# Performance work log

Hardware: AMD Instinct MI355X
Metric: run time of the kernel (lower is better)

Reference implementation:

```python
import jax, jax.numpy as jnp
import numpy as np

DIM = 256
MUL = 4
NUM_ENTRIES = 64
B, K = 16, 64
R = MUL * DIM


def setup_inputs() -> dict:
    key = jax.random.key(0)
    k_slots, k_idx, k_w1, k_w2 = jax.random.split(key, 4)
    slots = jax.random.normal(k_slots, (B, K, DIM), dtype=jnp.float32)
    indices = jax.random.randint(k_idx, (B, K), 0, NUM_ENTRIES, dtype=jnp.int64)
    # xavier_normal: std = sqrt(2 / (fan_in + fan_out)) over last two dims
    std1 = float(np.sqrt(2.0 / (DIM + R)))
    std2 = float(np.sqrt(2.0 / (R + DIM)))
    w1 = jax.random.normal(k_w1, (NUM_ENTRIES, DIM, R), dtype=jnp.float32) * std1
    w2 = jax.random.normal(k_w2, (NUM_ENTRIES, R, DIM), dtype=jnp.float32) * std2
    b1 = jnp.zeros((NUM_ENTRIES, R), dtype=jnp.float32)
    b2 = jnp.zeros((NUM_ENTRIES, DIM), dtype=jnp.float32)
    return {"slots": slots, "w1": w1, "b1": b1, "w2": w2, "b2": b2, "indices": indices}


def reference(slots, w1, b1, w2, b2, indices):
    # gather per-(b,k) expert weights, then 2-layer MLP (matvec per slot)
    h = jnp.einsum('bkd,bkdr->bkr', slots, w1[indices]) + b1[indices]  # (B,K,R)
    h = jax.nn.relu(h)
    out = jnp.einsum('bkr,bkrd->bkd', h, w2[indices]) + b2[indices]    # (B,K,DIM)
    return out
```

## Files before the change

### kernel.cpp

```cpp
#include <hip/hip_runtime.h>
#include <stdint.h>

#define DIMC 256
#define RTOT 1024
#define NE 64
#define NSLOT 1024
#define RCN 8
#define RCW 128
#define TILE 32
#define XSTR 264
#define NT 16

typedef short bfrag __attribute__((ext_vector_type(8)));
typedef float f32x4 __attribute__((ext_vector_type(4)));

#define VMCNT(N) asm volatile("s_waitcnt vmcnt(" #N ")" ::: "memory")
#define LGKM0_BAR()                                          \
  do {                                                       \
    asm volatile("s_waitcnt lgkmcnt(0)" ::: "memory");       \
    __builtin_amdgcn_s_barrier();                            \
  } while (0)

static __device__ __forceinline__ unsigned short f2bf(float f) {
  unsigned u = __float_as_uint(f);
  return (unsigned short)((u + 0x7FFFu + ((u >> 16) & 1u)) >> 16);
}

static __device__ __forceinline__ bfrag pack8(const float* f) {
  union { unsigned short u[8]; bfrag v; } r;
#pragma unroll
  for (int i = 0; i < 8; ++i) r.u[i] = f2bf(f[i]);
  return r.v;
}

static __device__ __forceinline__ void gload16(const float* g, float* l) {
  __builtin_amdgcn_global_load_lds(
      (const __attribute__((address_space(1))) void*)g,
      (__attribute__((address_space(3))) void*)l, 16, 0, 0);
}

template <int USE_WS>
__global__ __launch_bounds__(512, 4) void mlp_kernel(
    const float* __restrict__ slots, const float* __restrict__ w1,
    const float* __restrict__ b1, const float* __restrict__ w2,
    const float* __restrict__ b2, const int* __restrict__ indices,
    float* __restrict__ part, float* __restrict__ out) {
  const int e  = blockIdx.x;
  const int rc = blockIdx.y;
  const int t  = threadIdx.x;
  const int l  = t & 63;
  const int w  = t >> 6;
  const int ln = l & 15;
  const int kg = l >> 4;
  const int rbase = rc * RCW;

  __shared__ __align__(16) float WT[3][4096];
  __shared__ __align__(16) unsigned short X[TILE * XSTR];
  __shared__ unsigned short blist[NSLOT];
  __shared__ int sid[TILE];
  __shared__ int bn_s;

  if (t == 0) bn_s = 0;
  __syncthreads();
  {
    int i0 = indices[t] & (NE - 1);
    int i1 = indices[t + 512] & (NE - 1);
    if (i0 == e) { int p = atomicAdd(&bn_s, 1); blist[p] = (unsigned short)t; }
    if (i1 == e) { int p = atomicAdd(&bn_s, 1); blist[p] = (unsigned short)(t + 512); }
  }
  __syncthreads();
  const int n = bn_s;
  if (n == 0) return;

  const float* w1e = w1 + (size_t)e * DIMC * RTOT + rbase;
  const float* w2e = w2 + (size_t)e * RTOT * DIMC + (size_t)rbase * DIMC;
  const int   c    = w * 16 + ln;
  const float b1v  = b1[e * RTOT + rbase + c];
  float* prc = part + (size_t)rc * NSLOT * DIMC;

  auto STAGE = [&](int tt, float* buf) {
    if (tt < 8) {
      const float* g = w1e + (size_t)(tt * 32 + (t >> 5)) * RTOT + (t & 31) * 4;
      gload16(g, buf + t * 4);
      gload16(g + (size_t)16 * RTOT, buf + 2048 + t * 4);
    } else {
      const int rt = (tt - 8) >> 1, dh = tt & 1;
      const float* g =
          w2e + (size_t)(rt * 32 + (t >> 5)) * DIMC + dh * 128 + (t & 31) * 4;
      gload16(g, buf + t * 4);
      gload16(g + 16 * DIMC, buf + 2048 + t * 4);
    }
  };

  for (int s0 = 0; s0 < n; s0 += TILE) {
    const int m = (n - s0 < TILE) ? (n - s0) : TILE;

    LGKM0_BAR();
    if (t < TILE) sid[t] = (t < m) ? (int)blist[s0 + t] : 0;
    LGKM0_BAR();

#pragma unroll
    for (int i = t; i < TILE * 64; i += 512) {
      int s = i >> 6, d4 = (i & 63) * 4;
      float4 v = make_float4(0.f, 0.f, 0.f, 0.f);
      if (s < m) v = ((const float4*)slots)[(size_t)sid[s] * 64 + (i & 63)];
      union { unsigned short u[4]; uint2 q; } p;
      p.u[0] = f2bf(v.x); p.u[1] = f2bf(v.y);
      p.u[2] = f2bf(v.z); p.u[3] = f2bf(v.w);
      *(uint2*)&X[s * XSTR + d4] = p.q;
    }

    f32x4 acc1[2];
    acc1[0] = (f32x4)(0.f); acc1[1] = (f32x4)(0.f);
    f32x4 acc2[2][2];
#pragma unroll
    for (int mt = 0; mt < 2; ++mt)
#pragma unroll
      for (int dh = 0; dh < 2; ++dh) acc2[mt][dh] = (f32x4)(0.f);

    STAGE(0, WT[0]);
    STAGE(1, WT[1]);

#pragma unroll
    for (int tt = 0; tt < NT; ++tt) {
      if (tt < NT - 1) VMCNT(2);
      else             VMCNT(0);
      LGKM0_BAR();

      if (tt == 8) {
#pragma unroll
        for (int mt = 0; mt < 2; ++mt)
#pragma unroll
          for (int reg = 0; reg < 4; ++reg) {
            float h = fmaxf(acc1[mt][reg] + b1v, 0.f);
            X[(mt * 16 + kg * 4 + reg) * XSTR + c] = f2bf(h);
          }
        LGKM0_BAR();
      }

      if (tt + 2 < NT) STAGE(tt + 2, WT[(tt + 2) % 3]);

      {
        const float* buf = WT[tt % 3];
        float f[8];
#pragma unroll
        for (int j = 0; j < 8; ++j) f[j] = buf[(kg * 8 + j) * RCW + c];
        bfrag b = pack8(f);
        if (tt < 8) {
          bfrag a0 = *(const bfrag*)&X[ln * XSTR + tt * 32 + kg * 8];
          bfrag a1 = *(const bfrag*)&X[(16 + ln) * XSTR + tt * 32 + kg * 8];
          acc1[0] = __builtin_amdgcn_mfma_f32_16x16x32_bf16(a0, b, acc1[0], 0, 0, 0);
          acc1[1] = __builtin_amdgcn_mfma_f32_16x16x32_bf16(a1, b, acc1[1], 0, 0, 0);
        } else {
          const int rt = (tt - 8) >> 1, dh = tt & 1;
          bfrag a0 = *(const bfrag*)&X[ln * XSTR + rt * 32 + kg * 8];
          bfrag a1 = *(const bfrag*)&X[(16 + ln) * XSTR + rt * 32 + kg * 8];
          acc2[0][dh] = __builtin_amdgcn_mfma_f32_16x16x32_bf16(a0, b, acc2[0][dh], 0, 0, 0);
          acc2[1][dh] = __builtin_amdgcn_mfma_f32_16x16x32_bf16(a1, b, acc2[1][dh], 0, 0, 0);
        }
      }
    }

#pragma unroll
    for (int dh = 0; dh < 2; ++dh) {
      const int col = dh * 128 + c;
      const float b2v =
          (!USE_WS && rc == 0) ? b2[e * DIMC + col] : 0.f;
#pragma unroll
      for (int mt = 0; mt < 2; ++mt)
#pragma unroll
        for (int reg = 0; reg < 4; ++reg) {
          const int row = mt * 16 + kg * 4 + reg;
          if (row < m) {
            if (USE_WS) {
              prc[(size_t)sid[row] * DIMC + col] = acc2[mt][dh][reg];
            } else {
              atomicAdd(&out[(size_t)sid[row] * DIMC + col],
                        acc2[mt][dh][reg] + b2v);
            }
          }
        }
    }
  }
}

__global__ __launch_bounds__(256) void reduce_kernel(
    const float* __restrict__ part, const float* __restrict__ b2,
    const int* __restrict__ indices, float* __restrict__ out) {
  const int i = blockIdx.x * 256 + threadIdx.x;
  const int slot = i >> 6;
  const int e = indices[slot] & (NE - 1);
  f32x4 s = *(const f32x4*)(b2 + e * DIMC + (i & 63) * 4);
#pragma unroll
  for (int rc = 0; rc < RCN; ++rc)
    s += *(const f32x4*)(part + (size_t)rc * NSLOT * DIMC + (size_t)i * 4);
  *(f32x4*)(out + (size_t)i * 4) = s;
}

extern "C" void kernel_launch(void* const* d_in, const int* in_sizes, int n_in,
                              void* d_out, int out_size, void* d_ws, size_t ws_size,
                              hipStream_t stream) {
  const float* slots   = (const float*)d_in[0];
  const float* w1      = (const float*)d_in[1];
  const float* b1      = (const float*)d_in[2];
  const float* w2      = (const float*)d_in[3];
  const float* b2      = (const float*)d_in[4];
  const int*   indices = (const int*)d_in[5];
  float* out = (float*)d_out;

  const size_t need = (size_t)RCN * NSLOT * DIMC * sizeof(float);
  if (ws_size >= need) {
    float* part = (float*)d_ws;
    mlp_kernel<1><<<dim3(NE, RCN), 512, 0, stream>>>(slots, w1, b1, w2, b2,
                                                     indices, part, out);
    reduce_kernel<<<NSLOT * DIMC / 4 / 256, 256, 0, stream>>>(part, b2,
                                                              indices, out);
  } else {
    hipMemsetAsync(d_out, 0, (size_t)out_size * sizeof(float), stream);
    mlp_kernel<0><<<dim3(NE, RCN), 512, 0, stream>>>(slots, w1, b1, w2, b2,
                                                     indices, nullptr, out);
  }
}
```

Baseline: 163.2 us.

## Give each wave private weight staging with all loads issued upfront

Replaces the block-wide triple-buffered weight pipeline, which needed a barrier at every step, with a per-wave 16 KB LDS region. Each wave issues all of its w1 loads at once (and later all of its w2 loads) and waits on them with graded vmcnt counts, so block barriers are only needed around the X and hidden-activation exchanges. The layer-2 column split also changes so that each wave owns 32 output columns. LDS grows from 48 KB to 128 KB of weight buffers and the occupancy hint drops from 4 to 2, which trades latency hiding across blocks for deeper in-flight loads within each wave.

```diff
diff --git a/kernel.cpp b/kernel.cpp
--- a/kernel.cpp
+++ b/kernel.cpp
@@ -9,12 +9,11 @@
 #define RCW 128
 #define TILE 32
 #define XSTR 264
-#define NT 16
 
 typedef short bfrag __attribute__((ext_vector_type(8)));
 typedef float f32x4 __attribute__((ext_vector_type(4)));
 
-#define VMCNT(N) asm volatile("s_waitcnt vmcnt(" #N ")" ::: "memory")
+#define WAITV(n) asm volatile("s_waitcnt vmcnt(" #n ")" ::: "memory")
 #define LGKM0_BAR()                                          \
   do {                                                       \
     asm volatile("s_waitcnt lgkmcnt(0)" ::: "memory");       \
@@ -39,8 +38,23 @@
       (__attribute__((address_space(3))) void*)l, 16, 0, 0);
 }
 
+static __device__ __forceinline__ void waitv_l1(int ks) {
+  switch (ks) {
+    case 0: WAITV(14); break; case 1: WAITV(12); break;
+    case 2: WAITV(10); break; case 3: WAITV(8);  break;
+    case 4: WAITV(6);  break; case 5: WAITV(4);  break;
+    case 6: WAITV(2);  break; default: WAITV(0); break;
+  }
+}
+static __device__ __forceinline__ void waitv_l2(int rt) {
+  switch (rt) {
+    case 0: WAITV(12); break; case 1: WAITV(8); break;
+    case 2: WAITV(4);  break; default: WAITV(0); break;
+  }
+}
+
 template <int USE_WS>
-__global__ __launch_bounds__(512, 4) void mlp_kernel(
+__global__ __launch_bounds__(512, 2) void mlp_kernel(
     const float* __restrict__ slots, const float* __restrict__ w1,
     const float* __restrict__ b1, const float* __restrict__ w2,
     const float* __restrict__ b2, const int* __restrict__ indices,
@@ -54,7 +68,7 @@
   const int kg = l >> 4;
   const int rbase = rc * RCW;
 
-  __shared__ __align__(16) float WT[3][4096];
+  __shared__ __align__(16) float WB[8][4096];
   __shared__ __align__(16) unsigned short X[TILE * XSTR];
   __shared__ unsigned short blist[NSLOT];
   __shared__ int sid[TILE];
@@ -76,28 +90,18 @@
   const float* w2e = w2 + (size_t)e * RTOT * DIMC + (size_t)rbase * DIMC;
   const int   c    = w * 16 + ln;
   const float b1v  = b1[e * RTOT + rbase + c];
+  float* WBw = WB[w];
   float* prc = part + (size_t)rc * NSLOT * DIMC;
 
-  auto STAGE = [&](int tt, float* buf) {
-    if (tt < 8) {
-      const float* g = w1e + (size_t)(tt * 32 + (t >> 5)) * RTOT + (t & 31) * 4;
-      gload16(g, buf + t * 4);
-      gload16(g + (size_t)16 * RTOT, buf + 2048 + t * 4);
-    } else {
-      const int rt = (tt - 8) >> 1, dh = tt & 1;
-      const float* g =
-          w2e + (size_t)(rt * 32 + (t >> 5)) * DIMC + dh * 128 + (t & 31) * 4;
-      gload16(g, buf + t * 4);
-      gload16(g + 16 * DIMC, buf + 2048 + t * 4);
-    }
-  };
+  const int r4 = l >> 2, c4 = (l & 3) * 4;
+  const int r8 = l >> 3, c8 = (l & 7) * 4;
 
   for (int s0 = 0; s0 < n; s0 += TILE) {
     const int m = (n - s0 < TILE) ? (n - s0) : TILE;
 
-    LGKM0_BAR();
+    __syncthreads();
     if (t < TILE) sid[t] = (t < m) ? (int)blist[s0 + t] : 0;
-    LGKM0_BAR();
+    __syncthreads();
 
 #pragma unroll
     for (int i = t; i < TILE * 64; i += 512) {
@@ -109,63 +113,79 @@
       p.u[2] = f2bf(v.z); p.u[3] = f2bf(v.w);
       *(uint2*)&X[s * XSTR + d4] = p.q;
     }
+    __syncthreads();
+
+#pragma unroll
+    for (int ks = 0; ks < 8; ++ks)
+#pragma unroll
+      for (int hf = 0; hf < 2; ++hf) {
+        const float* src =
+            w1e + (size_t)(ks * 32 + hf * 16 + r4) * RTOT + w * 16 + c4;
+        gload16(src, WBw + ks * 512 + hf * 256 + l * 4);
+      }
 
     f32x4 acc1[2];
     acc1[0] = (f32x4)(0.f); acc1[1] = (f32x4)(0.f);
+#pragma unroll
+    for (int ks = 0; ks < 8; ++ks) {
+      waitv_l1(ks);
+      float f[8];
+#pragma unroll
+      for (int j = 0; j < 8; ++j) f[j] = WBw[ks * 512 + (kg * 8 + j) * 16 + ln];
+      bfrag b = pack8(f);
+      bfrag a0 = *(const bfrag*)&X[ln * XSTR + ks * 32 + kg * 8];
+      bfrag a1 = *(const bfrag*)&X[(16 + ln) * XSTR + ks * 32 + kg * 8];
+      acc1[0] = __builtin_amdgcn_mfma_f32_16x16x32_bf16(a0, b, acc1[0], 0, 0, 0);
+      acc1[1] = __builtin_amdgcn_mfma_f32_16x16x32_bf16(a1, b, acc1[1], 0, 0, 0);
+    }
+
+    asm volatile("s_waitcnt lgkmcnt(0)" ::: "memory");
+#pragma unroll
+    for (int rt = 0; rt < 4; ++rt)
+#pragma unroll
+      for (int q = 0; q < 4; ++q) {
+        const float* src =
+            w2e + (size_t)(rt * 32 + q * 8 + r8) * DIMC + w * 32 + c8;
+        gload16(src, WBw + rt * 1024 + q * 256 + l * 4);
+      }
+
+    LGKM0_BAR();
+
+#pragma unroll
+    for (int mt = 0; mt < 2; ++mt)
+#pragma unroll
+      for (int reg = 0; reg < 4; ++reg) {
+        float h = fmaxf(acc1[mt][reg] + b1v, 0.f);
+        X[(mt * 16 + kg * 4 + reg) * XSTR + c] = f2bf(h);
+      }
+    LGKM0_BAR();
+
     f32x4 acc2[2][2];
 #pragma unroll
     for (int mt = 0; mt < 2; ++mt)
 #pragma unroll
-      for (int dh = 0; dh < 2; ++dh) acc2[mt][dh] = (f32x4)(0.f);
-
-    STAGE(0, WT[0]);
-    STAGE(1, WT[1]);
-
-#pragma unroll
-    for (int tt = 0; tt < NT; ++tt) {
-      if (tt < NT - 1) VMCNT(2);
-      else             VMCNT(0);
-      LGKM0_BAR();
-
-      if (tt == 8) {
-#pragma unroll
-        for (int mt = 0; mt < 2; ++mt)
-#pragma unroll
-          for (int reg = 0; reg < 4; ++reg) {
-            float h = fmaxf(acc1[mt][reg] + b1v, 0.f);
-            X[(mt * 16 + kg * 4 + reg) * XSTR + c] = f2bf(h);
-          }
-        LGKM0_BAR();
-      }
-
-      if (tt + 2 < NT) STAGE(tt + 2, WT[(tt + 2) % 3]);
-
-      {
-        const float* buf = WT[tt % 3];
+      for (int nt = 0; nt < 2; ++nt) acc2[mt][nt] = (f32x4)(0.f);
+#pragma unroll
+    for (int rt = 0; rt < 4; ++rt) {
+      waitv_l2(rt);
+      bfrag a0 = *(const bfrag*)&X[ln * XSTR + rt * 32 + kg * 8];
+      bfrag a1 = *(const bfrag*)&X[(16 + ln) * XSTR + rt * 32 + kg * 8];
+#pragma unroll
+      for (int nt = 0; nt < 2; ++nt) {
         float f[8];
 #pragma unroll
-        for (int j = 0; j < 8; ++j) f[j] = buf[(kg * 8 + j) * RCW + c];
+        for (int j = 0; j < 8; ++j)
+          f[j] = WBw[rt * 1024 + (kg * 8 + j) * 32 + nt * 16 + ln];
         bfrag b = pack8(f);
-        if (tt < 8) {
-          bfrag a0 = *(const bfrag*)&X[ln * XSTR + tt * 32 + kg * 8];
-          bfrag a1 = *(const bfrag*)&X[(16 + ln) * XSTR + tt * 32 + kg * 8];
-          acc1[0] = __builtin_amdgcn_mfma_f32_16x16x32_bf16(a0, b, acc1[0], 0, 0, 0);
-          acc1[1] = __builtin_amdgcn_mfma_f32_16x16x32_bf16(a1, b, acc1[1], 0, 0, 0);
-        } else {
-          const int rt = (tt - 8) >> 1, dh = tt & 1;
-          bfrag a0 = *(const bfrag*)&X[ln * XSTR + rt * 32 + kg * 8];
-          bfrag a1 = *(const bfrag*)&X[(16 + ln) * XSTR + rt * 32 + kg * 8];
-          acc2[0][dh] = __builtin_amdgcn_mfma_f32_16x16x32_bf16(a0, b, acc2[0][dh], 0, 0, 0);
-          acc2[1][dh] = __builtin_amdgcn_mfma_f32_16x16x32_bf16(a1, b, acc2[1][dh], 0, 0, 0);
-        }
-      }
-    }
-
-#pragma unroll
-    for (int dh = 0; dh < 2; ++dh) {
-      const int col = dh * 128 + c;
-      const float b2v =
-          (!USE_WS && rc == 0) ? b2[e * DIMC + col] : 0.f;
+        acc2[0][nt] = __builtin_amdgcn_mfma_f32_16x16x32_bf16(a0, b, acc2[0][nt], 0, 0, 0);
+        acc2[1][nt] = __builtin_amdgcn_mfma_f32_16x16x32_bf16(a1, b, acc2[1][nt], 0, 0, 0);
+      }
+    }
+
+#pragma unroll
+    for (int nt = 0; nt < 2; ++nt) {
+      const int col = w * 32 + nt * 16 + ln;
+      const float b2v = (!USE_WS && rc == 0) ? b2[e * DIMC + col] : 0.f;
 #pragma unroll
       for (int mt = 0; mt < 2; ++mt)
 #pragma unroll
@@ -173,10 +193,10 @@
           const int row = mt * 16 + kg * 4 + reg;
           if (row < m) {
             if (USE_WS) {
-              prc[(size_t)sid[row] * DIMC + col] = acc2[mt][dh][reg];
+              prc[(size_t)sid[row] * DIMC + col] = acc2[mt][nt][reg];
             } else {
               atomicAdd(&out[(size_t)sid[row] * DIMC + col],
-                        acc2[mt][dh][reg] + b2v);
+                        acc2[mt][nt][reg] + b2v);
             }
           }
         }
```

Result: slower. 169.8 us (+4.0%).

## Fuse partial-sum reduction into MLP kernel via last-block counter

Applied to the files above, without the earlier changes.

Drops the separate reduce kernel. Each expert keeps a per-expert atomic counter in the workspace, and the last of its 8 r-chunk blocks sums the partials for that expert's slots, adds b2 and writes the output. The two weight-tile prefetches are also issued before the slot-to-bf16 conversion, so the load latency overlaps that work. This saves a kernel launch and a full pass over the partial buffer, but adds fences, a serialized tail on one block per expert, and a counter that is never reset and relies on the workspace starting at a multiple of 8.

```diff
diff --git a/kernel.cpp b/kernel.cpp
--- a/kernel.cpp
+++ b/kernel.cpp
@@ -44,7 +44,8 @@
     const float* __restrict__ slots, const float* __restrict__ w1,
     const float* __restrict__ b1, const float* __restrict__ w2,
     const float* __restrict__ b2, const int* __restrict__ indices,
-    float* __restrict__ part, float* __restrict__ out) {
+    float* __restrict__ part, int* __restrict__ done,
+    float* __restrict__ out) {
   const int e  = blockIdx.x;
   const int rc = blockIdx.y;
   const int t  = threadIdx.x;
@@ -59,6 +60,7 @@
   __shared__ unsigned short blist[NSLOT];
   __shared__ int sid[TILE];
   __shared__ int bn_s;
+  __shared__ int lastf;
 
   if (t == 0) bn_s = 0;
   __syncthreads();
@@ -99,6 +101,9 @@
     if (t < TILE) sid[t] = (t < m) ? (int)blist[s0 + t] : 0;
     LGKM0_BAR();
 
+    STAGE(0, WT[0]);
+    STAGE(1, WT[1]);
+
 #pragma unroll
     for (int i = t; i < TILE * 64; i += 512) {
       int s = i >> 6, d4 = (i & 63) * 4;
@@ -117,9 +122,6 @@
     for (int mt = 0; mt < 2; ++mt)
 #pragma unroll
       for (int dh = 0; dh < 2; ++dh) acc2[mt][dh] = (f32x4)(0.f);
-
-    STAGE(0, WT[0]);
-    STAGE(1, WT[1]);
 
 #pragma unroll
     for (int tt = 0; tt < NT; ++tt) {
@@ -164,8 +166,7 @@
 #pragma unroll
     for (int dh = 0; dh < 2; ++dh) {
       const int col = dh * 128 + c;
-      const float b2v =
-          (!USE_WS && rc == 0) ? b2[e * DIMC + col] : 0.f;
+      const float b2v = (!USE_WS && rc == 0) ? b2[e * DIMC + col] : 0.f;
 #pragma unroll
       for (int mt = 0; mt < 2; ++mt)
 #pragma unroll
@@ -182,19 +183,25 @@
         }
     }
   }
-}
-
-__global__ __launch_bounds__(256) void reduce_kernel(
-    const float* __restrict__ part, const float* __restrict__ b2,
-    const int* __restrict__ indices, float* __restrict__ out) {
-  const int i = blockIdx.x * 256 + threadIdx.x;
-  const int slot = i >> 6;
-  const int e = indices[slot] & (NE - 1);
-  f32x4 s = *(const f32x4*)(b2 + e * DIMC + (i & 63) * 4);
-#pragma unroll
-  for (int rc = 0; rc < RCN; ++rc)
-    s += *(const f32x4*)(part + (size_t)rc * NSLOT * DIMC + (size_t)i * 4);
-  *(f32x4*)(out + (size_t)i * 4) = s;
+
+  if (USE_WS) {
+    __threadfence();
+    if (t == 0) lastf = ((atomicAdd(&done[e], 1) & 7) == 7);
+    __syncthreads();
+    if (lastf) {
+      __threadfence();
+      for (int i = t; i < n * 64; i += 512) {
+        const int s  = blist[i >> 6];
+        const int c4 = i & 63;
+        f32x4 acc = *(const f32x4*)(b2 + e * DIMC + c4 * 4);
+#pragma unroll
+        for (int r2 = 0; r2 < RCN; ++r2)
+          acc += *(const f32x4*)(part + (size_t)r2 * NSLOT * DIMC +
+                                 (size_t)s * DIMC + c4 * 4);
+        *(f32x4*)(out + (size_t)s * DIMC + c4 * 4) = acc;
+      }
+    }
+  }
 }
 
 extern "C" void kernel_launch(void* const* d_in, const int* in_sizes, int n_in,
@@ -208,16 +215,16 @@
   const int*   indices = (const int*)d_in[5];
   float* out = (float*)d_out;
 
-  const size_t need = (size_t)RCN * NSLOT * DIMC * sizeof(float);
-  if (ws_size >= need) {
+  const size_t part_bytes = (size_t)RCN * NSLOT * DIMC * sizeof(float);
+  if (ws_size >= part_bytes + 256) {
     float* part = (float*)d_ws;
+    int*   done = (int*)((char*)d_ws + part_bytes);
     mlp_kernel<1><<<dim3(NE, RCN), 512, 0, stream>>>(slots, w1, b1, w2, b2,
-                                                     indices, part, out);
-    reduce_kernel<<<NSLOT * DIMC / 4 / 256, 256, 0, stream>>>(part, b2,
-                                                              indices, out);
+                                                     indices, part, done, out);
   } else {
     hipMemsetAsync(d_out, 0, (size_t)out_size * sizeof(float), stream);
     mlp_kernel<0><<<dim3(NE, RCN), 512, 0, stream>>>(slots, w1, b1, w2, b2,
-                                                     indices, nullptr, out);
-  }
-}
+                                                     indices, nullptr, nullptr,
+                                                     out);
+  }
+}
```

After: 296.5 us. +81.7%, slower.
